# Kernel optimization log

Hardware: AMD Instinct MI355X
Metric: run time of the kernel (lower is better)

## Reference

```python
import jax, jax.numpy as jnp
import numpy as np

# DMV constants (direction 0 = child left of head, per `direction = 0 if head_i > child_i`)
NC, HC, GO, STOP, LEFT, RIGHT = 0, 1, 0, 1, 0, 1
NEG = -1e9
B, N, T = 1024, 64, 64


def setup_inputs():
    key = jax.random.key(0)
    ks = jax.random.split(key, 6)
    tag_array = jax.random.randint(ks[0], (B, N), 0, T)
    # valid lengths in [N//2, N]
    len_array = jax.random.randint(ks[1], (B,), N // 2, N + 1)
    id_array = jnp.arange(B, dtype=jnp.int32)
    # parameters are log-probabilities in the original model; normalize for realism
    root_param = jax.nn.log_softmax(0.1 * jax.random.normal(ks[2], (T,), jnp.float32))
    trans_param = jax.nn.log_softmax(0.1 * jax.random.normal(ks[3], (T, T, 2, 1), jnp.float32), axis=1)
    dec_param = jax.nn.log_softmax(0.1 * jax.random.normal(ks[4], (T, 2, 2, 2), jnp.float32), axis=3)
    return dict(id_array=id_array, tag_array=tag_array, len_array=len_array,
                root_param=root_param, trans_param=trans_param, dec_param=dec_param)


def dmv_inside(root_param, trans_param, dec_param, tag_array, len_array):
    """Batched DMV inside algorithm (log space, sum semiring). Returns [B] log-likelihoods."""
    Bs, n = tag_array.shape
    lse = jax.nn.logsumexp
    th = tag_array
    tp = trans_param[..., 0]                                   # [T,T,2] (cv=1)
    trans_l = tp[th[:, :, None], th[:, None, :], LEFT]          # [B,h,m] attach m left of h
    trans_r = tp[th[:, :, None], th[:, None, :], RIGHT]         # [B,h,m] attach m right of h
    dec = dec_param[th]                                         # [B,n,dir,val,decision]
    goR_nc, goR_hc = dec[:, :, RIGHT, NC, GO], dec[:, :, RIGHT, HC, GO]
    goL_nc, goL_hc = dec[:, :, LEFT, NC, GO], dec[:, :, LEFT, HC, GO]
    stR_nc, stR_hc = dec[:, :, RIGHT, NC, STOP], dec[:, :, RIGHT, HC, STOP]
    stL_nc, stL_hc = dec[:, :, LEFT, NC, STOP], dec[:, :, LEFT, HC, STOP]
    root = root_param[th]                                       # [B,n]

    ar = jnp.arange(n)
    full = jnp.full((Bs, n, n), NEG, dtype=trans_r.dtype)
    # C*: half-constituent without STOP; F*: finished half-constituent (with STOP)
    CR = full.at[:, ar, ar].set(0.0)
    CL = full.at[:, ar, ar].set(0.0)
    FR = full.at[:, ar, ar].set(stR_nc)
    FL = full.at[:, ar, ar].set(stL_nc)
    IR = full
    IL = full

    for w in range(1, n):                                       # span width
        k = jnp.arange(w)
        # ---------- right direction: head h, span [h, e=h+w] ----------
        h = jnp.arange(n - w); e = h + w
        S = h[:, None] + k[None, :]                             # split s in [h, e-1]
        go = jnp.where(k[None, None, :] == 0, goR_nc[:, h, None], goR_hc[:, h, None])
        inner = CR[:, h[:, None], S] + go + FL[:, e[:, None], S + 1]
        ir = trans_r[:, h, e] + lse(inner, axis=-1)             # attach e as child of h
        IR = IR.at[:, h, e].set(ir)
        M = S + 1                                               # last child m in [h+1, e]
        cr = lse(IR[:, h[:, None], M] + FR[:, M, e[:, None]], axis=-1)
        CR = CR.at[:, h, e].set(cr)
        FR = FR.at[:, h, e].set(cr + stR_hc[:, h])
        # ---------- left direction: head h, span [m0=h-w, h] ----------
        hl = jnp.arange(w, n); m0 = hl - w
        S2 = hl[:, None] - k[None, :]                           # split s in [m0+1, h]
        go2 = jnp.where(k[None, None, :] == 0, goL_nc[:, hl, None], goL_hc[:, hl, None])
        inner2 = CL[:, hl[:, None], S2] + go2 + FR[:, m0[:, None], S2 - 1]
        il = trans_l[:, hl, m0] + lse(inner2, axis=-1)          # attach m0 as child of h
        IL = IL.at[:, hl, m0].set(il)
        M2 = S2 - 1                                             # last child m in [m0, h-1]
        cl = lse(IL[:, hl[:, None], M2] + FL[:, M2, m0[:, None]], axis=-1)
        CL = CL.at[:, hl, m0].set(cl)
        FL = FL.at[:, hl, m0].set(cl + stL_hc[:, hl])

    # root picks one head r covering [0, len-1]
    last = len_array - 1
    fr_end = FR[jnp.arange(Bs)[:, None], ar[None, :], last[:, None]]   # [B,n]
    score = root + FL[:, :, 0] + fr_end
    score = jnp.where(ar[None, :] < len_array[:, None], score, NEG)
    return lse(score, axis=-1)


def reference(id_array, tag_array, len_array, root_param, trans_param, dec_param):
    # forward() -> per-sentence inside log-probability ('sum' mode since e_step_mode='em')
    return dmv_inside(root_param, trans_param, dec_param, tag_array, len_array)
```

## Files before the change

### kernel.cpp

```cpp
#include <hip/hip_runtime.h>


#define NEGV   -1000000000.0f
#define NMAX   64
#define LDS_S  69
#define BLOCK  512
#define ALPHA  8.0f

#if __has_builtin(__builtin_amdgcn_exp2f)
#define EXP2F(x) __builtin_amdgcn_exp2f(x)
#else
#define EXP2F(x) __expf((x) * 0.6931471805599453f)
#endif
#if __has_builtin(__builtin_amdgcn_logf)
#define LOG2F(x) __builtin_amdgcn_logf(x)
#else
#define LOG2F(x) (__logf(x) * 1.4426950408889634f)
#endif
#define LOG2E 1.4426950408889634f
#define LN2   0.6931471805599453f

template<int CTRL>
__device__ __forceinline__ float dppf(float v) {
    return __int_as_float(__builtin_amdgcn_update_dpp(
        0, __float_as_int(v), CTRL, 0xF, 0xF, true));
}
__device__ __forceinline__ float grp8_sum(float s) {
    s += dppf<0xB1>(s);
    s += dppf<0x4E>(s);
    s += dppf<0x141>(s);
    return s;
}

__global__ void order_kernel(const int* __restrict__ len_arr,
                             int* __restrict__ blk2item, int B)
{
    __shared__ int hist[33];
    __shared__ int base[33];
    const int tid = threadIdx.x;
    if (tid < 33) hist[tid] = 0;
    __syncthreads();
    int bin = 0;
    if (tid < B) {
        bin = 64 - len_arr[tid];
        atomicAdd(&hist[bin], 1);
    }
    __syncthreads();
    if (tid == 0) {
        int acc = 0;
        for (int i = 0; i < 33; ++i) { base[i] = acc; acc += hist[i]; }
    }
    __syncthreads();
    if (tid < B) {
        int rank = atomicAdd(&base[bin], 1);
        int j;
        if ((B & 255) == 0) {
            int q = rank >> 8, pos = rank & 255;
            j = (q & 1) ? ((q << 8) + 255 - pos) : ((q << 8) + pos);
        } else {
            j = rank;
        }
        blk2item[j] = tid;
    }
}

template<int NJ>
__device__ __forceinline__ void dmv_step(
    const int w, const int cd, const int gid, const int lg,
    float* __restrict__ sI, float* __restrict__ sF,
    const float* __restrict__ goNCl, const float* __restrict__ goHMl,
    const float* __restrict__ stHCl, const float* __restrict__ stNCl,
    const int* __restrict__ th_s, const float* __restrict__ trans_param)
{
    if (gid >= cd) return;
    const int h = gid, e = h + w;

    const int thh = th_s[h], the = th_s[e];
    const float trlR = EXP2F(trans_param[(thh * NMAX + the) * 2 + 1] * LOG2E + ALPHA);
    const float trlL = EXP2F(trans_param[(the * NMAX + thh) * 2 + 0] * LOG2E + ALPHA);
    const float gncR = goNCl[NMAX + h], gmR = goHMl[NMAX + h];
    const float gncL = goNCl[e],        gmL = goHMl[e];
    const float dcR  = stNCl[NMAX + h];
    const float dcL  = stNCl[e];
    const float dcRe = stNCl[NMAX + e];
    const float dcLh = stNCl[h];

    const int pF = h * LDS_S + h;
    const int pC = e * LDS_S + h + 1;
    float sInt = 0.f, bndR = 0.f, bndL = 0.f;
    #pragma unroll
    for (int j = 0; j < NJ; ++j) {
        const int k = lg + 8 * j;
        if (j == NJ - 1) {
            const int kc = (k < w) ? k : (w - 1);
            float vF = sF[pF + kc];
            float vC = sF[pC + kc];
            float tR = ((k == 0) ? gncR : vF * gmR) * ((k == w - 1) ? dcL : vC);
            float tL = ((k == w - 1) ? gncL : vC * gmL) * ((k == 0) ? dcR : vF);
            bndR += (k < w) ? tR : 0.f;
            bndL += (k < w) ? tL : 0.f;
        } else if (j == 0) {
            float vF = sF[pF + k];
            float vC = sF[pC + k];
            bndR += ((k == 0) ? gncR : vF * gmR) * vC;
            bndL += (vC * gmL) * ((k == 0) ? dcR : vF);
        } else {
            sInt = fmaf(sF[pF + k], sF[pC + k], sInt);
        }
    }
    const float aR = grp8_sum(fmaf(gmR, sInt, bndR));
    const float aL = grp8_sum(fmaf(gmL, sInt, bndL));
    const float irR = trlR * aR;
    const float irL = trlL * aL;
    if (lg == 0) sI[h * LDS_S + e] = irR;
    if (lg == 1) sI[e * LDS_S + h] = irL;

    const int pIR = h * LDS_S + h + 1;
    const int pGR = (h + 1) * LDS_S + e;
    const int pIL = e * LDS_S + h;
    const int pGL = h * LDS_S + h;
    float accR = 0.f, accL = 0.f;
    #pragma unroll
    for (int j = 0; j < NJ; ++j) {
        const int k = lg + 8 * j;
        if (j == NJ - 1) {
            const int kc = (k < w) ? k : (w - 1);
            float i1 = sI[pIR + kc];
            float f1 = sF[pGR + kc * LDS_S];
            float i2 = sI[pIL + kc];
            float f2 = sF[pGL + kc * LDS_S];
            float tR = ((k == w - 1) ? irR : i1) * ((k == w - 1) ? dcRe : f1);
            float tL = ((k == 0) ? irL : i2) * ((k == 0) ? dcLh : f2);
            accR += (k < w) ? tR : 0.f;
            accL += (k < w) ? tL : 0.f;
        } else if (j == 0) {
            float i1 = sI[pIR + k];
            float f1 = sF[pGR + k * LDS_S];
            float i2 = sI[pIL + k];
            float f2 = sF[pGL + k * LDS_S];
            accR = fmaf(i1, f1, accR);
            accL += ((k == 0) ? irL : i2) * ((k == 0) ? dcLh : f2);
        } else {
            accR = fmaf(sI[pIR + k], sF[pGR + k * LDS_S], accR);
            accL = fmaf(sI[pIL + k], sF[pGL + k * LDS_S], accL);
        }
    }
    const float bR = grp8_sum(accR);
    const float bL = grp8_sum(accL);
    if (lg == 0) sF[h * LDS_S + e] = stHCl[NMAX + h] * bR;
    if (lg == 1) sF[e * LDS_S + h] = stHCl[e] * bL;
}

__global__ __launch_bounds__(BLOCK, 8)
void dmv_inside_kernel(const int* __restrict__ tag,
                       const int* __restrict__ len_arr,
                       const float* __restrict__ root_param,
                       const float* __restrict__ trans_param,
                       const float* __restrict__ dec_param,
                       const int* __restrict__ blk2item,
                       float* __restrict__ out)
{
    __shared__ float sI[NMAX * LDS_S];
    __shared__ float sF[NMAX * LDS_S];
    __shared__ float goNCl[2 * NMAX];
    __shared__ float goHMl[2 * NMAX];
    __shared__ float stHCl[2 * NMAX];
    __shared__ float stNCl[2 * NMAX];
    __shared__ float root_l[NMAX];
    __shared__ int   th_s[NMAX];

    const int b   = blk2item[blockIdx.x];
    const int tid = threadIdx.x;
    const int nl  = len_arr[b];

    if (tid < NMAX) {
        int t = tag[b * NMAX + tid];
        th_s[tid] = t;
        const float* d = dec_param + t * 8;
        goNCl[0 * NMAX + tid] = EXP2F(d[0] * LOG2E);
        stNCl[0 * NMAX + tid] = EXP2F(d[1] * LOG2E);
        goHMl[0 * NMAX + tid] = EXP2F((d[2] - d[3]) * LOG2E);
        stHCl[0 * NMAX + tid] = EXP2F(d[3] * LOG2E);
        goNCl[1 * NMAX + tid] = EXP2F(d[4] * LOG2E);
        stNCl[1 * NMAX + tid] = EXP2F(d[5] * LOG2E);
        goHMl[1 * NMAX + tid] = EXP2F((d[6] - d[7]) * LOG2E);
        stHCl[1 * NMAX + tid] = EXP2F(d[7] * LOG2E);
        root_l[tid]           = EXP2F(root_param[t] * LOG2E);
    }
    __syncthreads();

    const int gid = tid >> 3;
    const int lg  = tid & 7;

    for (int w = 1; w < nl; ++w) {
        const int cd = nl - w;
        switch ((w - 1) >> 3) {
        case 0: dmv_step<1>(w, cd, gid, lg, sI, sF, goNCl, goHMl, stHCl, stNCl, th_s, trans_param); break;
        case 1: dmv_step<2>(w, cd, gid, lg, sI, sF, goNCl, goHMl, stHCl, stNCl, th_s, trans_param); break;
        case 2: dmv_step<3>(w, cd, gid, lg, sI, sF, goNCl, goHMl, stHCl, stNCl, th_s, trans_param); break;
        case 3: dmv_step<4>(w, cd, gid, lg, sI, sF, goNCl, goHMl, stHCl, stNCl, th_s, trans_param); break;
        case 4: dmv_step<5>(w, cd, gid, lg, sI, sF, goNCl, goHMl, stHCl, stNCl, th_s, trans_param); break;
        case 5: dmv_step<6>(w, cd, gid, lg, sI, sF, goNCl, goHMl, stHCl, stNCl, th_s, trans_param); break;
        case 6: dmv_step<7>(w, cd, gid, lg, sI, sF, goNCl, goHMl, stHCl, stNCl, th_s, trans_param); break;
        default: dmv_step<8>(w, cd, gid, lg, sI, sF, goNCl, goHMl, stHCl, stNCl, th_s, trans_param); break;
        }
        __syncthreads();
    }

    if (tid < 64) {
        const int last = nl - 1;
        float fl0 = (tid == 0)    ? stNCl[0 * NMAX + 0]    : sF[tid * LDS_S + 0];
        float fre = (tid == last) ? stNCl[1 * NMAX + last] : sF[tid * LDS_S + last];
        float xx  = (tid < nl) ? (root_l[tid] * fl0 * fre) : 0.f;
        #pragma unroll
        for (int off = 1; off < 64; off <<= 1)
            xx += __shfl_xor(xx, off, 64);
        if (tid == 0) out[b] = (LOG2F(xx) - ALPHA * last) * LN2;
    }
}

extern "C" void kernel_launch(void* const* d_in, const int* in_sizes, int n_in,
                              void* d_out, int out_size, void* d_ws, size_t ws_size,
                              hipStream_t stream) {
    const int*   tag   = (const int*)d_in[1];
    const int*   len_a = (const int*)d_in[2];
    const float* root  = (const float*)d_in[3];
    const float* trans = (const float*)d_in[4];
    const float* dec   = (const float*)d_in[5];
    float* outp = (float*)d_out;
    const int B = in_sizes[2];

    int* blk2item = (int*)d_ws;

    int sortThreads = (B < 1024) ? ((B + 63) & ~63) : 1024;
    if (sortThreads < 64) sortThreads = 64;
    order_kernel<<<1, sortThreads, 0, stream>>>(len_a, blk2item, B);
    dmv_inside_kernel<<<B, BLOCK, 0, stream>>>(tag, len_a, root, trans, dec,
                                               blk2item, outp);
}
```

Measured before the change: 55.10 us.

## Cache each head's row of F and I spans in registers across span widths

Each 8-lane group owns a fixed head h across all widths, so the row values sF[h][h+k] and sI[h][h+k] it produces are now kept in per-thread register arrays (fS, iS) instead of being reread from LDS. The step function becomes a macro so those arrays stay in registers across the width loop. The second reduction is reindexed by child position, with the boundary term folded in as irR*dcRe outside the loop. This cuts LDS reads in the inner loops at the cost of 16 extra registers and more intricate ownership logic for which lane stores each element.

```diff
diff --git a/kernel.cpp b/kernel.cpp
--- a/kernel.cpp
+++ b/kernel.cpp
@@ -64,92 +64,82 @@
     }
 }
 
-template<int NJ>
-__device__ __forceinline__ void dmv_step(
-    const int w, const int cd, const int gid, const int lg,
-    float* __restrict__ sI, float* __restrict__ sF,
-    const float* __restrict__ goNCl, const float* __restrict__ goHMl,
-    const float* __restrict__ stHCl, const float* __restrict__ stNCl,
-    const int* __restrict__ th_s, const float* __restrict__ trans_param)
-{
-    if (gid >= cd) return;
-    const int h = gid, e = h + w;
-
-    const int thh = th_s[h], the = th_s[e];
-    const float trlR = EXP2F(trans_param[(thh * NMAX + the) * 2 + 1] * LOG2E + ALPHA);
-    const float trlL = EXP2F(trans_param[(the * NMAX + thh) * 2 + 0] * LOG2E + ALPHA);
-    const float gncR = goNCl[NMAX + h], gmR = goHMl[NMAX + h];
-    const float gncL = goNCl[e],        gmL = goHMl[e];
-    const float dcR  = stNCl[NMAX + h];
-    const float dcL  = stNCl[e];
-    const float dcRe = stNCl[NMAX + e];
-    const float dcLh = stNCl[h];
-
-    const int pF = h * LDS_S + h;
-    const int pC = e * LDS_S + h + 1;
-    float sInt = 0.f, bndR = 0.f, bndL = 0.f;
-    #pragma unroll
-    for (int j = 0; j < NJ; ++j) {
-        const int k = lg + 8 * j;
-        if (j == NJ - 1) {
-            const int kc = (k < w) ? k : (w - 1);
-            float vF = sF[pF + kc];
-            float vC = sF[pC + kc];
-            float tR = ((k == 0) ? gncR : vF * gmR) * ((k == w - 1) ? dcL : vC);
-            float tL = ((k == w - 1) ? gncL : vC * gmL) * ((k == 0) ? dcR : vF);
-            bndR += (k < w) ? tR : 0.f;
-            bndL += (k < w) ? tL : 0.f;
-        } else if (j == 0) {
-            float vF = sF[pF + k];
-            float vC = sF[pC + k];
-            bndR += ((k == 0) ? gncR : vF * gmR) * vC;
-            bndL += (vC * gmL) * ((k == 0) ? dcR : vF);
-        } else {
-            sInt = fmaf(sF[pF + k], sF[pC + k], sInt);
-        }
-    }
-    const float aR = grp8_sum(fmaf(gmR, sInt, bndR));
-    const float aL = grp8_sum(fmaf(gmL, sInt, bndL));
-    const float irR = trlR * aR;
-    const float irL = trlL * aL;
-    if (lg == 0) sI[h * LDS_S + e] = irR;
-    if (lg == 1) sI[e * LDS_S + h] = irL;
-
-    const int pIR = h * LDS_S + h + 1;
-    const int pGR = (h + 1) * LDS_S + e;
-    const int pIL = e * LDS_S + h;
-    const int pGL = h * LDS_S + h;
-    float accR = 0.f, accL = 0.f;
-    #pragma unroll
-    for (int j = 0; j < NJ; ++j) {
-        const int k = lg + 8 * j;
-        if (j == NJ - 1) {
-            const int kc = (k < w) ? k : (w - 1);
-            float i1 = sI[pIR + kc];
-            float f1 = sF[pGR + kc * LDS_S];
-            float i2 = sI[pIL + kc];
-            float f2 = sF[pGL + kc * LDS_S];
-            float tR = ((k == w - 1) ? irR : i1) * ((k == w - 1) ? dcRe : f1);
-            float tL = ((k == 0) ? irL : i2) * ((k == 0) ? dcLh : f2);
-            accR += (k < w) ? tR : 0.f;
-            accL += (k < w) ? tL : 0.f;
-        } else if (j == 0) {
-            float i1 = sI[pIR + k];
-            float f1 = sF[pGR + k * LDS_S];
-            float i2 = sI[pIL + k];
-            float f2 = sF[pGL + k * LDS_S];
-            accR = fmaf(i1, f1, accR);
-            accL += ((k == 0) ? irL : i2) * ((k == 0) ? dcLh : f2);
-        } else {
-            accR = fmaf(sI[pIR + k], sF[pGR + k * LDS_S], accR);
-            accL = fmaf(sI[pIL + k], sF[pGL + k * LDS_S], accL);
-        }
-    }
-    const float bR = grp8_sum(accR);
-    const float bL = grp8_sum(accL);
-    if (lg == 0) sF[h * LDS_S + e] = stHCl[NMAX + h] * bR;
-    if (lg == 1) sF[e * LDS_S + h] = stHCl[e] * bL;
-}
+#define DMV_STEP(NJ)                                                          \
+  {                                                                           \
+    const int cd = nl - w;                                                    \
+    if (gid < cd) {                                                           \
+      const int h = gid, e = h + w;                                           \
+      const int thh = th_s[h], the = th_s[e];                                 \
+      const float trlR = EXP2F(trans_param[(thh * NMAX + the) * 2 + 1] * LOG2E + ALPHA); \
+      const float trlL = EXP2F(trans_param[(the * NMAX + thh) * 2 + 0] * LOG2E + ALPHA); \
+      const float gncR = goNCl[NMAX + h], gmR = goHMl[NMAX + h];              \
+      const float gncL = goNCl[e],        gmL = goHMl[e];                     \
+      const float dcR  = stNCl[NMAX + h], dcL = stNCl[e];                     \
+      const float dcRe = stNCl[NMAX + e], dcLh = stNCl[h];                    \
+      const int pC = e * LDS_S + h + 1;                                       \
+      float sInt = 0.f, bndR = 0.f, bndL = 0.f;                               \
+      _Pragma("unroll")                                                       \
+      for (int j = 0; j < (NJ); ++j) {                                        \
+        const int k = lg + 8 * j;                                             \
+        if (j == (NJ) - 1) {                                                  \
+          const int kc = (k < w) ? k : (w - 1);                               \
+          const float vC = sF[pC + kc];                                       \
+          const float vF = fS[j];                                             \
+          const float tR = ((k == 0) ? gncR : vF * gmR) * ((k == w - 1) ? dcL : vC); \
+          const float tL = ((k == w - 1) ? gncL : vC * gmL) * ((k == 0) ? dcR : vF); \
+          bndR += (k < w) ? tR : 0.f;                                         \
+          bndL += (k < w) ? tL : 0.f;                                         \
+        } else if (j == 0) {                                                  \
+          const float vC = sF[pC + k];                                        \
+          const float vF = fS[0];                                             \
+          bndR += ((k == 0) ? gncR : vF * gmR) * vC;                          \
+          bndL += (vC * gmL) * ((k == 0) ? dcR : vF);                         \
+        } else {                                                              \
+          sInt = fmaf(fS[j], sF[pC + k], sInt);                               \
+        }                                                                     \
+      }                                                                       \
+      const float aR = grp8_sum(fmaf(gmR, sInt, bndR));                       \
+      const float aL = grp8_sum(fmaf(gmL, sInt, bndL));                       \
+      const float irR = trlR * aR;                                            \
+      const float irL = trlL * aL;                                            \
+      if (lg == 1) sI[e * LDS_S + h] = irL;                                   \
+      if ((NJ) < 8 && w == 8 * (NJ)) {                                        \
+        if (lg == 0) iS[((NJ) < 8) ? (NJ) : 0] = irR;                         \
+      } else {                                                                \
+        if (lg == (w & 7)) iS[(NJ) - 1] = irR;                                \
+      }                                                                       \
+      const int pGR = h * LDS_S + e;                                          \
+      const int pIL = e * LDS_S + h;                                          \
+      const int pGL = h * LDS_S + h;                                          \
+      float accR = 0.f, accL = 0.f;                                           \
+      _Pragma("unroll")                                                       \
+      for (int j = 0; j < (NJ); ++j) {                                        \
+        const int m = lg + 8 * j;                                             \
+        if (j == 0 || j == (NJ) - 1) {                                        \
+          const bool ok = (m >= 1) && (m <= w - 1);                           \
+          const int mc = ok ? m : 1;                                          \
+          const float tR = iS[j] * sF[pGR + mc * LDS_S];                      \
+          const float tL = sI[pIL + mc] * sF[pGL + mc * LDS_S];               \
+          accR += ok ? tR : 0.f;                                              \
+          accL += ok ? tL : 0.f;                                              \
+        } else {                                                              \
+          accR = fmaf(iS[j], sF[pGR + m * LDS_S], accR);                      \
+          accL = fmaf(sI[pIL + m], sF[pGL + m * LDS_S], accL);                \
+        }                                                                     \
+      }                                                                       \
+      const float bR = grp8_sum(accR) + irR * dcRe;                           \
+      const float bL = grp8_sum(accL) + irL * dcLh;                           \
+      const float fR = stHCl[NMAX + h] * bR;                                  \
+      const float fL = stHCl[e] * bL;                                         \
+      if (lg == 0) sF[h * LDS_S + e] = fR;                                    \
+      if (lg == 1) sF[e * LDS_S + h] = fL;                                    \
+      if ((NJ) < 8 && w == 8 * (NJ)) {                                        \
+        if (lg == 0) fS[((NJ) < 8) ? (NJ) : 0] = fR;                          \
+      } else {                                                                \
+        if (lg == (w & 7)) fS[(NJ) - 1] = fR;                                 \
+      }                                                                       \
+    }                                                                         \
+  }
 
 __global__ __launch_bounds__(BLOCK, 8)
 void dmv_inside_kernel(const int* __restrict__ tag,
@@ -192,17 +182,20 @@
     const int gid = tid >> 3;
     const int lg  = tid & 7;
 
+    float fS[8], iS[8];
+    #pragma unroll
+    for (int i = 0; i < 8; ++i) { fS[i] = 0.f; iS[i] = 0.f; }
+
     for (int w = 1; w < nl; ++w) {
-        const int cd = nl - w;
         switch ((w - 1) >> 3) {
-        case 0: dmv_step<1>(w, cd, gid, lg, sI, sF, goNCl, goHMl, stHCl, stNCl, th_s, trans_param); break;
-        case 1: dmv_step<2>(w, cd, gid, lg, sI, sF, goNCl, goHMl, stHCl, stNCl, th_s, trans_param); break;
-        case 2: dmv_step<3>(w, cd, gid, lg, sI, sF, goNCl, goHMl, stHCl, stNCl, th_s, trans_param); break;
-        case 3: dmv_step<4>(w, cd, gid, lg, sI, sF, goNCl, goHMl, stHCl, stNCl, th_s, trans_param); break;
-        case 4: dmv_step<5>(w, cd, gid, lg, sI, sF, goNCl, goHMl, stHCl, stNCl, th_s, trans_param); break;
-        case 5: dmv_step<6>(w, cd, gid, lg, sI, sF, goNCl, goHMl, stHCl, stNCl, th_s, trans_param); break;
-        case 6: dmv_step<7>(w, cd, gid, lg, sI, sF, goNCl, goHMl, stHCl, stNCl, th_s, trans_param); break;
-        default: dmv_step<8>(w, cd, gid, lg, sI, sF, goNCl, goHMl, stHCl, stNCl, th_s, trans_param); break;
+        case 0: DMV_STEP(1); break;
+        case 1: DMV_STEP(2); break;
+        case 2: DMV_STEP(3); break;
+        case 3: DMV_STEP(4); break;
+        case 4: DMV_STEP(5); break;
+        case 5: DMV_STEP(6); break;
+        case 6: DMV_STEP(7); break;
+        default: DMV_STEP(8); break;
         }
         __syncthreads();
     }
```

After: 66.31 us. 20.3% more time.
